# Optimization experiments

Measured on AMD Instinct MI355X. Metric: run time of the kernel, lower is better.

## Reference

```python
import jax, jax.numpy as jnp
import numpy as np

RADIUS = 0.2
NSAMPLE = 32
USE_XYZ = True

B, N, NPOINT, C = 4, 16384, 2048, 64


def setup_inputs() -> dict:
    key = jax.random.key(0)
    k1, k2, k3 = jax.random.split(key, 3)
    xyz = jax.random.uniform(k1, (B, N, 3), dtype=jnp.float32)
    new_xyz = jax.random.uniform(k2, (B, NPOINT, 3), dtype=jnp.float32)
    features = jax.random.normal(k3, (B, C, N), dtype=jnp.float32)
    return {"xyz": xyz, "new_xyz": new_xyz, "features": features}


def _ball_query(radius, nsample, xyz, new_xyz):
    # xyz: (B,N,3), new_xyz: (B,S,3) -> idx: (B,S,nsample) int32
    d2 = jnp.sum((new_xyz[:, :, None, :] - xyz[:, None, :, :]) ** 2, axis=-1)  # (B,S,N)
    mask = d2 < radius * radius
    # stable sort puts in-ball indices first, preserving original order
    order = jnp.argsort(~mask, axis=-1, stable=True)  # (B,S,N)
    idx = order[..., :nsample]  # first nsample in-ball indices (or fillers)
    count = jnp.sum(mask, axis=-1, dtype=jnp.int32)  # (B,S)
    slot_valid = jnp.arange(nsample, dtype=jnp.int32)[None, None, :] < count[..., None]
    # pad with the first valid index (index 0 if the ball is empty),
    # matching the reference CUDA ball_query behavior
    idx = jnp.where(slot_valid, idx, idx[..., :1])
    return idx.astype(jnp.int32)


def _group(features, idx):
    # features: (B,C,N), idx: (B,S,K) -> (B,C,S,K)
    return jnp.take_along_axis(features[:, :, None, :], idx[:, None, :, :], axis=3)


def reference(xyz, new_xyz, features):
    idx = _ball_query(RADIUS, NSAMPLE, xyz, new_xyz)  # (B,S,K)
    xyz_t = jnp.transpose(xyz, (0, 2, 1))  # (B,3,N)
    grouped_xyz = _group(xyz_t, idx)  # (B,3,S,K)
    grouped_xyz = grouped_xyz - jnp.transpose(new_xyz, (0, 2, 1))[..., None]
    grouped_features = _group(features, idx)  # (B,C,S,K)
    if USE_XYZ:
        new_features = jnp.concatenate([grouped_xyz, grouped_features], axis=1)
    else:
        new_features = grouped_features
    return new_features  # (B, 3+C, S, K)
```

## Files before the change

kernel.cpp:

```cpp
#include <hip/hip_runtime.h>


namespace {
constexpr int kN   = 16384;
constexpr int kNP  = 2048;
constexpr int kC   = 64;
constexpr int kNS  = 32;
constexpr int kOC  = 3 + kC;
constexpr int kWin = 256;
}

__device__ __forceinline__ float d2_rn(float nx, float ny, float nz,
                                       float px, float py, float pz) {
    const float dx = __fsub_rn(nx, px);
    const float dy = __fsub_rn(ny, py);
    const float dz = __fsub_rn(nz, pz);
    return __fadd_rn(__fadd_rn(__fmul_rn(dx, dx), __fmul_rn(dy, dy)),
                     __fmul_rn(dz, dz));
}

__global__ __launch_bounds__(256) void prep_kernel(
    const float* __restrict__ xyz,
    const float* __restrict__ new_xyz,
    const float* __restrict__ feat,
    float* __restrict__ tf,
    int*   __restrict__ idxbuf)
{
    __shared__ float tile[64][65];
    __shared__ int   sIdx[4][kNS];

    const int t = threadIdx.x;

    if (blockIdx.x < 1024) {
        const int b  = blockIdx.x >> 8;
        const int n0 = (blockIdx.x & 255) << 6;
        const float* fb = feat + (size_t)b * kC * kN;
        float* ob       = tf   + (size_t)b * kN * kC;
        const int q  = t >> 6;
        const int nn = t & 63;
        #pragma unroll
        for (int p = 0; p < 16; ++p) {
            const int c = p * 4 + q;
            tile[c][nn] = fb[(size_t)c * kN + n0 + nn];
        }
        __syncthreads();
        const int cc = t & 63;
        #pragma unroll
        for (int p = 0; p < 16; ++p) {
            const int n = p * 4 + q;
            ob[(size_t)(n0 + n) * kC + cc] = tile[cc][n];
        }
        return;
    }

    const int w = t >> 6;
    const int l = t & 63;
    const int qid = (blockIdx.x - 1024) * 4 + w;
    const int b   = qid >> 11;
    const int j   = qid & 2047;

    const float4* __restrict__ xv =
        reinterpret_cast<const float4*>(xyz + (size_t)b * kN * 3);
    const float* nxp = new_xyz + ((size_t)b * kNP + j) * 3;
    const float nx = nxp[0], ny = nxp[1], nz = nxp[2];
    const float R2 = 0.04f;

    int count = 0;
    float4 A0, A1, A2, B0, B1, B2;
    {
        const int o = 3 * l;
        B0 = xv[o]; B1 = xv[o + 1]; B2 = xv[o + 2];
    }
    for (int base = 0; base < kN; base += kWin) {
        A0 = B0; A1 = B1; A2 = B2;
        if (base + kWin < kN) {
            const int o = ((base + kWin) >> 2) * 3 + 3 * l;
            B0 = xv[o]; B1 = xv[o + 1]; B2 = xv[o + 2];
        }
        const float d0  = d2_rn(nx, ny, nz, A0.x, A0.y, A0.z);
        const float d1  = d2_rn(nx, ny, nz, A0.w, A1.x, A1.y);
        const float d2v = d2_rn(nx, ny, nz, A1.z, A1.w, A2.x);
        const float d3  = d2_rn(nx, ny, nz, A2.y, A2.z, A2.w);
        const unsigned long long b0 = __ballot(d0  < R2);
        const unsigned long long b1 = __ballot(d1  < R2);
        const unsigned long long b2 = __ballot(d2v < R2);
        const unsigned long long b3 = __ballot(d3  < R2);

        const unsigned long long m = (1ull << l) - 1ull;
        int slot = count + (int)(__popcll(b0 & m) + __popcll(b1 & m) +
                                 __popcll(b2 & m) + __popcll(b3 & m));
        const int i0 = base + 4 * l;
        if (d0  < R2) { if (slot < kNS) sIdx[w][slot] = i0 + 0; ++slot; }
        if (d1  < R2) { if (slot < kNS) sIdx[w][slot] = i0 + 1; ++slot; }
        if (d2v < R2) { if (slot < kNS) sIdx[w][slot] = i0 + 2; ++slot; }
        if (d3  < R2) { if (slot < kNS) sIdx[w][slot] = i0 + 3; ++slot; }

        count += (int)(__popcll(b0) + __popcll(b1) +
                       __popcll(b2) + __popcll(b3));
        if (count >= kNS) break;
    }
    __builtin_amdgcn_wave_barrier();

    if (count == 0) {
        if (l < kNS) sIdx[w][l] = 0;
    } else if (count < kNS) {
        const int first = sIdx[w][0];
        __builtin_amdgcn_wave_barrier();
        if (l >= count && l < kNS) sIdx[w][l] = first;
    }
    __builtin_amdgcn_wave_barrier();

    if (l < kNS) idxbuf[(size_t)qid * kNS + l] = sIdx[w][l];
}

__global__ __launch_bounds__(256) void gather_kernel(
    const float* __restrict__ xyz,
    const float* __restrict__ new_xyz,
    const float* __restrict__ tf,
    const int*   __restrict__ idxbuf,
    float* __restrict__ out)
{
    const int t = threadIdx.x;
    const int w = t >> 6;
    const int l = t & 63;

    const int bid = blockIdx.x;
    const int xcd = bid & 7;
    const int b   = xcd >> 1;
    const int jbl = ((xcd & 1) << 8) | (bid >> 3);
    const int j   = (jbl << 2) | w;
    const int qid = (b << 11) | j;

    const int s = l & 31;
    const int h = l >> 5;
    const int id = idxbuf[(size_t)qid * kNS + s];

    const float* __restrict__ xb = xyz + (size_t)b * kN * 3;
    const float* nxp = new_xyz + ((size_t)b * kNP + j) * 3;
    const float nx = nxp[0], ny = nxp[1], nz = nxp[2];

    const size_t cs = (size_t)kNP * kNS;
    float* ob = out + ((size_t)b * kOC * kNP + j) * kNS + s;

    if (h == 0) {
        const float g0 = xb[(size_t)id * 3 + 0] - nx;
        const float g1 = xb[(size_t)id * 3 + 1] - ny;
        const float g2 = xb[(size_t)id * 3 + 2] - nz;
        ob[0 * cs] = g0;
        ob[1 * cs] = g1;
        ob[2 * cs] = g2;
    }

    const float* row = tf + ((size_t)b * kN + id) * kC;
    float* obf = ob + 3 * cs;
    #pragma unroll
    for (int it = 0; it < 8; ++it) {
        const int chunk = it * 2 + h;
        const float4 v = *reinterpret_cast<const float4*>(row + chunk * 4);
        const size_t c0 = (size_t)chunk * 4;
        obf[(c0 + 0) * cs] = v.x;
        obf[(c0 + 1) * cs] = v.y;
        obf[(c0 + 2) * cs] = v.z;
        obf[(c0 + 3) * cs] = v.w;
    }
}

__global__ __launch_bounds__(256) void qg_direct(
    const float* __restrict__ xyz, const float* __restrict__ new_xyz,
    const float* __restrict__ feat, float* __restrict__ out)
{
    __shared__ int sIdx[4][kNS];
    const int wave = threadIdx.x >> 6;
    const int lane = threadIdx.x & 63;
    const int bid  = blockIdx.x;
    const int xcd  = bid & 7;
    const int b    = xcd >> 1;
    const int jblk = ((xcd & 1) << 8) | (bid >> 3);
    const int j    = (jblk << 2) | wave;

    const float* __restrict__ xb = xyz + (size_t)b * kN * 3;
    const float* nxp = new_xyz + ((size_t)b * kNP + j) * 3;
    const float nx = nxp[0], ny = nxp[1], nz = nxp[2];
    const float R2 = 0.04f;

    int count = 0;
    for (int base = 0; base < kN; base += 64) {
        const int i = base + lane;
        const float d2 = d2_rn(nx, ny, nz, xb[(size_t)i * 3 + 0],
                               xb[(size_t)i * 3 + 1], xb[(size_t)i * 3 + 2]);
        const bool in = d2 < R2;
        const unsigned long long bal = __ballot(in);
        const int pre  = (int)__popcll(bal & ((1ull << lane) - 1ull));
        const int slot = count + pre;
        if (in && slot < kNS) sIdx[wave][slot] = i;
        count += (int)__popcll(bal);
        if (count >= kNS) break;
    }
    __builtin_amdgcn_wave_barrier();
    if (count == 0) {
        if (lane < kNS) sIdx[wave][lane] = 0;
    } else if (count < kNS) {
        const int first = sIdx[wave][0];
        __builtin_amdgcn_wave_barrier();
        if (lane >= count && lane < kNS) sIdx[wave][lane] = first;
    }
    __builtin_amdgcn_wave_barrier();

    const int s    = lane & 31;
    const int half = lane >> 5;
    const int id   = sIdx[wave][s];
    const float g0 = xb[(size_t)id * 3 + 0] - nx;
    const float g1 = xb[(size_t)id * 3 + 1] - ny;
    const float g2 = xb[(size_t)id * 3 + 2] - nz;
    const size_t cs = (size_t)kNP * kNS;
    float* ob = out + (((size_t)b * kOC) * kNP + j) * kNS + s;
    const float* fb = feat + ((size_t)b * kC) * kN + id;
    #pragma unroll
    for (int cb = 0; cb < kOC; cb += 2) {
        const int c = cb + half;
        if (c < kOC) {
            float v;
            if (c < 3) v = (c == 0) ? g0 : ((c == 1) ? g1 : g2);
            else       v = fb[(size_t)(c - 3) * kN];
            ob[(size_t)c * cs] = v;
        }
    }
}

extern "C" void kernel_launch(void* const* d_in, const int* in_sizes, int n_in,
                              void* d_out, int out_size, void* d_ws, size_t ws_size,
                              hipStream_t stream) {
    const float* xyz     = (const float*)d_in[0];
    const float* new_xyz = (const float*)d_in[1];
    const float* feat    = (const float*)d_in[2];
    float* out           = (float*)d_out;

    const size_t tf_bytes  = (size_t)4 * kN * kC * sizeof(float);
    const size_t idx_bytes = (size_t)4 * kNP * kNS * sizeof(int);
    if (ws_size >= tf_bytes + idx_bytes) {
        float* tf   = (float*)d_ws;
        int* idxbuf = (int*)((char*)d_ws + tf_bytes);
        prep_kernel  <<<dim3(3072), dim3(256), 0, stream>>>(
            xyz, new_xyz, feat, tf, idxbuf);
        gather_kernel<<<dim3(2048), dim3(256), 0, stream>>>(
            xyz, new_xyz, tf, idxbuf, out);
    } else {
        qg_direct<<<dim3(2048), dim3(256), 0, stream>>>(xyz, new_xyz, feat, out);
    }
}
```

Before: 110.7 us.

## Fuse ball query into gather kernel and use nontemporal loads/stores

Ball query moves out of the prep kernel and into the gather kernel, so the neighbor indices stay in shared memory instead of going through a global index buffer. The prep kernel now only transposes the features. The output stores and the feature loads in the transpose become nontemporal, to reduce cache pollution from the streaming output. The trade-off is that the transpose no longer overlaps with the ball query inside one launch, and the gather now waits on each wave's search.

```diff
diff --git a/kernel.cpp b/kernel.cpp
--- a/kernel.cpp
+++ b/kernel.cpp
@@ -19,48 +19,50 @@
                      __fmul_rn(dz, dz));
 }
 
-__global__ __launch_bounds__(256) void prep_kernel(
+__global__ __launch_bounds__(256) void tr_kernel(
+    const float* __restrict__ feat, float* __restrict__ tf)
+{
+    __shared__ float tile[64][65];
+    const int b  = blockIdx.x >> 8;
+    const int n0 = (blockIdx.x & 255) << 6;
+    const float* fb = feat + (size_t)b * kC * kN;
+    float* ob       = tf   + (size_t)b * kN * kC;
+    const int t  = threadIdx.x;
+    const int q  = t >> 6;
+    const int nn = t & 63;
+    #pragma unroll
+    for (int p = 0; p < 16; ++p) {
+        const int c = p * 4 + q;
+        tile[c][nn] = __builtin_nontemporal_load(&fb[(size_t)c * kN + n0 + nn]);
+    }
+    __syncthreads();
+    const int cc = t & 63;
+    #pragma unroll
+    for (int p = 0; p < 16; ++p) {
+        const int n = p * 4 + q;
+        ob[(size_t)(n0 + n) * kC + cc] = tile[cc][n];
+    }
+}
+
+__global__ __launch_bounds__(256) void qg_fused(
     const float* __restrict__ xyz,
     const float* __restrict__ new_xyz,
-    const float* __restrict__ feat,
-    float* __restrict__ tf,
-    int*   __restrict__ idxbuf)
+    const float* __restrict__ tf,
+    float* __restrict__ out)
 {
-    __shared__ float tile[64][65];
-    __shared__ int   sIdx[4][kNS];
-
+    __shared__ int sIdx[4][kNS];
     const int t = threadIdx.x;
-
-    if (blockIdx.x < 1024) {
-        const int b  = blockIdx.x >> 8;
-        const int n0 = (blockIdx.x & 255) << 6;
-        const float* fb = feat + (size_t)b * kC * kN;
-        float* ob       = tf   + (size_t)b * kN * kC;
-        const int q  = t >> 6;
-        const int nn = t & 63;
-        #pragma unroll
-        for (int p = 0; p < 16; ++p) {
-            const int c = p * 4 + q;
-            tile[c][nn] = fb[(size_t)c * kN + n0 + nn];
-        }
-        __syncthreads();
-        const int cc = t & 63;
-        #pragma unroll
-        for (int p = 0; p < 16; ++p) {
-            const int n = p * 4 + q;
-            ob[(size_t)(n0 + n) * kC + cc] = tile[cc][n];
-        }
-        return;
-    }
-
     const int w = t >> 6;
     const int l = t & 63;
-    const int qid = (blockIdx.x - 1024) * 4 + w;
-    const int b   = qid >> 11;
-    const int j   = qid & 2047;
-
-    const float4* __restrict__ xv =
-        reinterpret_cast<const float4*>(xyz + (size_t)b * kN * 3);
+
+    const int bid = blockIdx.x;
+    const int xcd = bid & 7;
+    const int b   = xcd >> 1;
+    const int jbl = ((xcd & 1) << 8) | (bid >> 3);
+    const int j   = (jbl << 2) | w;
+
+    const float* __restrict__ xb = xyz + (size_t)b * kN * 3;
+    const float4* __restrict__ xv = reinterpret_cast<const float4*>(xb);
     const float* nxp = new_xyz + ((size_t)b * kNP + j) * 3;
     const float nx = nxp[0], ny = nxp[1], nz = nxp[2];
     const float R2 = 0.04f;
@@ -110,34 +112,9 @@
     }
     __builtin_amdgcn_wave_barrier();
 
-    if (l < kNS) idxbuf[(size_t)qid * kNS + l] = sIdx[w][l];
-}
-
-__global__ __launch_bounds__(256) void gather_kernel(
-    const float* __restrict__ xyz,
-    const float* __restrict__ new_xyz,
-    const float* __restrict__ tf,
-    const int*   __restrict__ idxbuf,
-    float* __restrict__ out)
-{
-    const int t = threadIdx.x;
-    const int w = t >> 6;
-    const int l = t & 63;
-
-    const int bid = blockIdx.x;
-    const int xcd = bid & 7;
-    const int b   = xcd >> 1;
-    const int jbl = ((xcd & 1) << 8) | (bid >> 3);
-    const int j   = (jbl << 2) | w;
-    const int qid = (b << 11) | j;
-
     const int s = l & 31;
     const int h = l >> 5;
-    const int id = idxbuf[(size_t)qid * kNS + s];
-
-    const float* __restrict__ xb = xyz + (size_t)b * kN * 3;
-    const float* nxp = new_xyz + ((size_t)b * kNP + j) * 3;
-    const float nx = nxp[0], ny = nxp[1], nz = nxp[2];
+    const int id = sIdx[w][s];
 
     const size_t cs = (size_t)kNP * kNS;
     float* ob = out + ((size_t)b * kOC * kNP + j) * kNS + s;
@@ -146,9 +123,9 @@
         const float g0 = xb[(size_t)id * 3 + 0] - nx;
         const float g1 = xb[(size_t)id * 3 + 1] - ny;
         const float g2 = xb[(size_t)id * 3 + 2] - nz;
-        ob[0 * cs] = g0;
-        ob[1 * cs] = g1;
-        ob[2 * cs] = g2;
+        __builtin_nontemporal_store(g0, &ob[0 * cs]);
+        __builtin_nontemporal_store(g1, &ob[1 * cs]);
+        __builtin_nontemporal_store(g2, &ob[2 * cs]);
     }
 
     const float* row = tf + ((size_t)b * kN + id) * kC;
@@ -158,10 +135,10 @@
         const int chunk = it * 2 + h;
         const float4 v = *reinterpret_cast<const float4*>(row + chunk * 4);
         const size_t c0 = (size_t)chunk * 4;
-        obf[(c0 + 0) * cs] = v.x;
-        obf[(c0 + 1) * cs] = v.y;
-        obf[(c0 + 2) * cs] = v.z;
-        obf[(c0 + 3) * cs] = v.w;
+        __builtin_nontemporal_store(v.x, &obf[(c0 + 0) * cs]);
+        __builtin_nontemporal_store(v.y, &obf[(c0 + 1) * cs]);
+        __builtin_nontemporal_store(v.z, &obf[(c0 + 2) * cs]);
+        __builtin_nontemporal_store(v.w, &obf[(c0 + 3) * cs]);
     }
 }
 
@@ -235,15 +212,11 @@
     const float* feat    = (const float*)d_in[2];
     float* out           = (float*)d_out;
 
-    const size_t tf_bytes  = (size_t)4 * kN * kC * sizeof(float);
-    const size_t idx_bytes = (size_t)4 * kNP * kNS * sizeof(int);
-    if (ws_size >= tf_bytes + idx_bytes) {
-        float* tf   = (float*)d_ws;
-        int* idxbuf = (int*)((char*)d_ws + tf_bytes);
-        prep_kernel  <<<dim3(3072), dim3(256), 0, stream>>>(
-            xyz, new_xyz, feat, tf, idxbuf);
-        gather_kernel<<<dim3(2048), dim3(256), 0, stream>>>(
-            xyz, new_xyz, tf, idxbuf, out);
+    const size_t tf_bytes = (size_t)4 * kN * kC * sizeof(float);
+    if (ws_size >= tf_bytes) {
+        float* tf = (float*)d_ws;
+        tr_kernel<<<dim3(1024), dim3(256), 0, stream>>>(feat, tf);
+        qg_fused <<<dim3(2048), dim3(256), 0, stream>>>(xyz, new_xyz, tf, out);
     } else {
         qg_direct<<<dim3(2048), dim3(256), 0, stream>>>(xyz, new_xyz, feat, out);
     }
```

New measurement: 108.5 us (median of 2 runs). 2.0% less time.
